# Performance work log

Measured on AMD Instinct MI355X. Metric: run time of the kernel, lower is better.

## Reference

```python
import jax, jax.numpy as jnp
import numpy as np

N_CLASSES = 256
GT_CLASSES = 21
DIM = 384
EPS = 1e-12  # matches torch F.normalize default eps


def setup_inputs() -> dict:
    key = jax.random.key(0)
    k1, k2, k3 = jax.random.split(key, 3)
    features = jax.random.normal(k1, (4, 256, 256, DIM), dtype=jnp.float32)
    weight = jax.random.uniform(k2, (4, 256, 256), dtype=jnp.float32)
    cluster_centers = jax.random.normal(k3, (N_CLASSES, DIM), dtype=jnp.float32)
    pseudo_assignment = (jnp.arange(N_CLASSES) % GT_CLASSES).astype(jnp.int32)
    return {
        "features": features,
        "weight": weight,
        "cluster_centers": cluster_centers,
        "pseudo_assignment": pseudo_assignment,
    }


def _l2norm(x, axis):
    # torch F.normalize: x / max(||x||, eps)
    n = jnp.sqrt(jnp.sum(x * x, axis=axis, keepdims=True))
    return x / jnp.maximum(n, EPS)


def reference(features, weight, cluster_centers, pseudo_assignment):
    lead_shape = features.shape[:-1]
    feats = features.reshape(-1, features.shape[-1])        # [N, D]
    w = weight.reshape(-1)                                   # [N]

    normed_clusters = _l2norm(cluster_centers, axis=1)       # [K, D]
    normed_features = _l2norm(feats, axis=1)                 # [N, D]

    inner_products = normed_features @ normed_clusters.T     # [N, K]
    class_labels = jnp.argmax(inner_products, axis=1)        # [N]

    # -(one_hot(labels) * inner_products).sum(1) == -inner_products[n, labels[n]]
    cluster_loss = -jnp.take_along_axis(
        inner_products, class_labels[:, None], axis=1
    )[:, 0]                                                  # [N]

    loss = jnp.mean(cluster_loss * w)

    pseudo_segs_pred = class_labels.reshape(lead_shape)
    segs_pred = pseudo_assignment[pseudo_segs_pred].astype(jnp.int64)
    return pseudo_segs_pred, segs_pred, loss
```

## Files before the change

kernel.cpp:

```cpp
#include <hip/hip_runtime.h>
#include <hip/hip_bf16.h>

#define NTOT (4*256*256)
#define DIM 384
#define KCL 256
#define BM 64
#define TBS 256
#define GRID_MAIN (NTOT/BM)
#define NT 12
#define EPS 1e-12f

#define AHI    0
#define ALO    4096
#define BH_OFF 8192
#define BL_OFF 24576
#define SMEM_BYTES 40960

typedef __attribute__((ext_vector_type(8))) _Float16 f16x8;
typedef __attribute__((ext_vector_type(4))) float f32x4;

__device__ __forceinline__ void async_copy16(const void* gptr, void* lptr) {
    __builtin_amdgcn_global_load_lds(
        (const __attribute__((address_space(1))) unsigned int*)gptr,
        (__attribute__((address_space(3))) unsigned int*)lptr, 16, 0, 0);
}

__global__ void prep_clusters(const float* __restrict__ cc,
                              _Float16* __restrict__ bh,
                              _Float16* __restrict__ bl) {
    int j = blockIdx.x, l = threadIdx.x;
    float v[6]; float ssq = 0.f;
#pragma unroll
    for (int i = 0; i < 6; ++i) { v[i] = cc[j*DIM + l + 64*i]; ssq = fmaf(v[i], v[i], ssq); }
#pragma unroll
    for (int off = 32; off >= 1; off >>= 1) ssq += __shfl_xor(ssq, off);
    float inv = 1.f / fmaxf(sqrtf(ssq), EPS);
    const int w = j >> 6, n = (j >> 4) & 3, nl = j & 15;
#pragma unroll
    for (int i = 0; i < 6; ++i) {
        int d = l + 64 * i;
        float x = v[i] * inv;
        _Float16 h  = (_Float16)x;
        _Float16 lo = (_Float16)(x - (float)h);
        size_t idx = (size_t)((((((d >> 5)*4 + w)*4 + n)*4 + ((d >> 3) & 3))*16 + nl)*8
                              + (d & 7));
        bh[idx] = h;
        bl[idx] = lo;
    }
}

__global__ __launch_bounds__(TBS, 3)
void kmeans_main(const float* __restrict__ A,
                 const float* __restrict__ W,
                 const _Float16* __restrict__ Bh,
                 const _Float16* __restrict__ Bl,
                 const int*   __restrict__ PA,
                 float* __restrict__ out,
                 float* __restrict__ partial)
{
    __shared__ unsigned char smem[SMEM_BYTES];

    const int tid  = threadIdx.x;
    const int wv   = tid >> 6;
    const int lane = tid & 63;
    const int g    = lane >> 4;
    const int l15  = lane & 15;
    const int sw   = (l15 >> 1) & 3;
    const int row0 = blockIdx.x * BM;
    const int arow = tid >> 2, achk = tid & 3;
    const int awb  = (((arow << 2) + (achk ^ ((arow >> 1) & 3))) << 4);
    const int fa   = l15 * 64 + ((g ^ sw) << 4);
    const int fb   = wv * 4096 + lane * 16;

    const float* ap = A + (size_t)(row0 + arow) * DIM + achk * 8;
    const unsigned char* bsh = (const unsigned char*)Bh + (size_t)(wv * 4) * 1024 + lane * 16;
    const unsigned char* bsl = (const unsigned char*)Bl + (size_t)(wv * 4) * 1024 + lane * 16;

    f32x4 acc[4][4];
#pragma unroll
    for (int m = 0; m < 4; ++m)
#pragma unroll
        for (int n = 0; n < 4; ++n) acc[m][n] = (f32x4){0.f, 0.f, 0.f, 0.f};
    float ssq = 0.f;

    auto stageB = [&](int t) {
#pragma unroll
        for (int n = 0; n < 4; ++n) {
            async_copy16(bsh + (size_t)(t * 16 + n) * 1024, smem + BH_OFF + fb + n * 1024);
            async_copy16(bsl + (size_t)(t * 16 + n) * 1024, smem + BL_OFF + fb + n * 1024);
        }
    };
    auto writeA = [&](const float4& x0, const float4& x1) {
        float av[8] = {x0.x, x0.y, x0.z, x0.w, x1.x, x1.y, x1.z, x1.w};
        f16x8 h8, l8;
#pragma unroll
        for (int e = 0; e < 8; ++e) {
            _Float16 hh = (_Float16)av[e];
            h8[e] = hh;
            l8[e] = (_Float16)(av[e] - (float)hh);
            ssq = fmaf(av[e], av[e], ssq);
        }
        *(f16x8*)(smem + AHI + awb) = h8;
        *(f16x8*)(smem + ALO + awb) = l8;
    };

    float4 rA0x, rA0y, rA1x, rA1y;

    rA0x = *(const float4*)(ap);
    rA0y = *(const float4*)(ap + 4);
    stageB(0);
    writeA(rA0x, rA0y);
    rA1x = *(const float4*)(ap + 32);
    rA1y = *(const float4*)(ap + 32 + 4);
    asm volatile("s_waitcnt lgkmcnt(0)" ::: "memory");
    __builtin_amdgcn_s_barrier();

#pragma unroll
    for (int t = 0; t < NT; ++t) {
        if (t < NT - 1) asm volatile("s_waitcnt vmcnt(2)" ::: "memory");
        else            asm volatile("s_waitcnt vmcnt(0)" ::: "memory");

        f16x8 ahf[4], alf[4], bfh[4], bfl[4];
#pragma unroll
        for (int m = 0; m < 4; ++m) {
            ahf[m] = *(const f16x8*)(smem + AHI + fa + m * 1024);
            alf[m] = *(const f16x8*)(smem + ALO + fa + m * 1024);
        }
#pragma unroll
        for (int n = 0; n < 4; ++n) {
            bfh[n] = *(const f16x8*)(smem + BH_OFF + fb + n * 1024);
            bfl[n] = *(const f16x8*)(smem + BL_OFF + fb + n * 1024);
        }
        asm volatile("s_waitcnt lgkmcnt(0)" ::: "memory");
        __builtin_amdgcn_s_barrier();

        if (t < NT - 1) {
            if (((t + 1) & 1) == 0) writeA(rA0x, rA0y); else writeA(rA1x, rA1y);
            stageB(t + 1);
            if (t + 2 < NT) {
                if (((t + 2) & 1) == 0) {
                    rA0x = *(const float4*)(ap + (t + 2) * 32);
                    rA0y = *(const float4*)(ap + (t + 2) * 32 + 4);
                } else {
                    rA1x = *(const float4*)(ap + (t + 2) * 32);
                    rA1y = *(const float4*)(ap + (t + 2) * 32 + 4);
                }
            }
        }

        __builtin_amdgcn_s_setprio(1);
#pragma unroll
        for (int m = 0; m < 4; ++m)
#pragma unroll
            for (int n = 0; n < 4; ++n)
                acc[m][n] = __builtin_amdgcn_mfma_f32_16x16x32_f16(ahf[m], bfh[n], acc[m][n], 0, 0, 0);
#pragma unroll
        for (int m = 0; m < 4; ++m)
#pragma unroll
            for (int n = 0; n < 4; ++n)
                acc[m][n] = __builtin_amdgcn_mfma_f32_16x16x32_f16(ahf[m], bfl[n], acc[m][n], 0, 0, 0);
#pragma unroll
        for (int m = 0; m < 4; ++m)
#pragma unroll
            for (int n = 0; n < 4; ++n)
                acc[m][n] = __builtin_amdgcn_mfma_f32_16x16x32_f16(alf[m], bfh[n], acc[m][n], 0, 0, 0);
        __builtin_amdgcn_s_setprio(0);

        if (t < NT - 1) {
            asm volatile("s_waitcnt lgkmcnt(0)" ::: "memory");
            __builtin_amdgcn_s_barrier();
        }
    }
    __syncthreads();

    float* rowssq = (float*)smem;
    float* wvalp  = (float*)(smem + 256);
    int*   wcolp  = (int*)(smem + 1280);

    ssq += __shfl_xor(ssq, 1);
    ssq += __shfl_xor(ssq, 2);
    if (achk == 0) rowssq[arow] = ssq;

#pragma unroll
    for (int m = 0; m < 4; ++m) {
#pragma unroll
        for (int j = 0; j < 4; ++j) {
            float best = acc[m][0][j];
            int   bc   = 64*wv + l15;
#pragma unroll
            for (int n = 1; n < 4; ++n) {
                float v = acc[m][n][j];
                int   c = 64*wv + 16*n + l15;
                if (v > best) { best = v; bc = c; }
            }
#pragma unroll
            for (int off = 1; off < 16; off <<= 1) {
                float ov = __shfl_xor(best, off);
                int   oc = __shfl_xor(bc, off);
                if (ov > best || (ov == best && oc < bc)) { best = ov; bc = oc; }
            }
            if (l15 == 0) {
                wvalp[wv * BM + 16*m + 4*g + j] = best;
                wcolp[wv * BM + 16*m + 4*g + j] = bc;
            }
        }
    }
    __syncthreads();

    if (tid < BM) {
        int r = tid;
        float best = wvalp[r]; int bc = wcolp[r];
#pragma unroll
        for (int w = 1; w < 4; ++w) {
            float ov = wvalp[w * BM + r]; int oc = wcolp[w * BM + r];
            if (ov > best || (ov == best && oc < bc)) { best = ov; bc = oc; }
        }
        float inv = 1.f / fmaxf(sqrtf(rowssq[r]), EPS);
        int gr = row0 + r;
        out[gr]        = (float)bc;
        out[NTOT + gr] = (float)PA[bc];
        float lsum = -(best * inv) * W[gr];
#pragma unroll
        for (int off = 32; off >= 1; off >>= 1) lsum += __shfl_xor(lsum, off);
        if (tid == 0) partial[blockIdx.x] = lsum;
    }
}

__global__ void loss_reduce(const float* __restrict__ partial, float* __restrict__ out_loss) {
    __shared__ float s[256];
    float v = 0.f;
    for (int i = threadIdx.x; i < GRID_MAIN; i += 256) v += partial[i];
    s[threadIdx.x] = v;
    __syncthreads();
    for (int off = 128; off >= 1; off >>= 1) {
        if ((int)threadIdx.x < off) s[threadIdx.x] += s[threadIdx.x + off];
        __syncthreads();
    }
    if (threadIdx.x == 0) out_loss[0] = s[0] * (1.0f / (float)NTOT);
}

extern "C" void kernel_launch(void* const* d_in, const int* in_sizes, int n_in,
                              void* d_out, int out_size, void* d_ws, size_t ws_size,
                              hipStream_t stream) {
    const float* features = (const float*)d_in[0];
    const float* weight   = (const float*)d_in[1];
    const float* cc       = (const float*)d_in[2];
    const int*   pa       = (const int*)d_in[3];
    float* out = (float*)d_out;

    _Float16* bh   = (_Float16*)d_ws;
    _Float16* bl   = bh + KCL * DIM;
    float* partial = (float*)(bl + KCL * DIM);

    hipLaunchKernelGGL(prep_clusters, dim3(KCL), dim3(64), 0, stream, cc, bh, bl);
    hipLaunchKernelGGL(kmeans_main, dim3(GRID_MAIN), dim3(TBS), 0, stream,
                       features, weight, bh, bl, pa, out, partial);
    hipLaunchKernelGGL(loss_reduce, dim3(1), dim3(256), 0, stream, partial, out + 2 * NTOT);
}
```

Measured before the change: 202.3 us.

## Load cluster fragments directly to registers and double-buffer A tile in LDS

The B operand (cluster hi/lo fp16 fragments) is no longer staged through LDS via async global-to-LDS copies; each wave loads its fragments straight into registers and prefetches the next tile's B halves between MFMA groups. A is double-buffered in LDS, which removes one barrier per iteration and cuts LDS from 40KB to 16KB. Launch bounds drop from 3 to 2 waves-per-EU minimum to allow the extra registers, which may reduce occupancy, and the direct global loads of B could add latency exposure.

```diff
diff --git a/kernel.cpp b/kernel.cpp
--- a/kernel.cpp
+++ b/kernel.cpp
@@ -10,20 +10,11 @@
 #define NT 12
 #define EPS 1e-12f
 
-#define AHI    0
-#define ALO    4096
-#define BH_OFF 8192
-#define BL_OFF 24576
-#define SMEM_BYTES 40960
+#define AB(p) ((p) * 8192)
+#define SMEM_BYTES 16384
 
 typedef __attribute__((ext_vector_type(8))) _Float16 f16x8;
 typedef __attribute__((ext_vector_type(4))) float f32x4;
-
-__device__ __forceinline__ void async_copy16(const void* gptr, void* lptr) {
-    __builtin_amdgcn_global_load_lds(
-        (const __attribute__((address_space(1))) unsigned int*)gptr,
-        (__attribute__((address_space(3))) unsigned int*)lptr, 16, 0, 0);
-}
 
 __global__ void prep_clusters(const float* __restrict__ cc,
                               _Float16* __restrict__ bh,
@@ -49,7 +40,7 @@
     }
 }
 
-__global__ __launch_bounds__(TBS, 3)
+__global__ __launch_bounds__(TBS, 2)
 void kmeans_main(const float* __restrict__ A,
                  const float* __restrict__ W,
                  const _Float16* __restrict__ Bh,
@@ -70,7 +61,6 @@
     const int arow = tid >> 2, achk = tid & 3;
     const int awb  = (((arow << 2) + (achk ^ ((arow >> 1) & 3))) << 4);
     const int fa   = l15 * 64 + ((g ^ sw) << 4);
-    const int fb   = wv * 4096 + lane * 16;
 
     const float* ap = A + (size_t)(row0 + arow) * DIM + achk * 8;
     const unsigned char* bsh = (const unsigned char*)Bh + (size_t)(wv * 4) * 1024 + lane * 16;
@@ -83,15 +73,26 @@
         for (int n = 0; n < 4; ++n) acc[m][n] = (f32x4){0.f, 0.f, 0.f, 0.f};
     float ssq = 0.f;
 
-    auto stageB = [&](int t) {
-#pragma unroll
-        for (int n = 0; n < 4; ++n) {
-            async_copy16(bsh + (size_t)(t * 16 + n) * 1024, smem + BH_OFF + fb + n * 1024);
-            async_copy16(bsl + (size_t)(t * 16 + n) * 1024, smem + BL_OFF + fb + n * 1024);
-        }
-    };
-    auto writeA = [&](const float4& x0, const float4& x1) {
-        float av[8] = {x0.x, x0.y, x0.z, x0.w, x1.x, x1.y, x1.z, x1.w};
+    f16x8  bfh[4], bfl[4];
+    float4 sA[2][2];
+
+    auto LDA = [&](int s, int tt) {
+        sA[s][0] = *(const float4*)(ap + tt * 32);
+        sA[s][1] = *(const float4*)(ap + tt * 32 + 4);
+    };
+    auto LDBH = [&](int tt) {
+#pragma unroll
+        for (int n = 0; n < 4; ++n)
+            bfh[n] = *(const f16x8*)(bsh + (size_t)(tt * 16 + n) * 1024);
+    };
+    auto LDBL = [&](int tt) {
+#pragma unroll
+        for (int n = 0; n < 4; ++n)
+            bfl[n] = *(const f16x8*)(bsl + (size_t)(tt * 16 + n) * 1024);
+    };
+    auto CVTW = [&](int s, int p) {
+        float av[8] = {sA[s][0].x, sA[s][0].y, sA[s][0].z, sA[s][0].w,
+                       sA[s][1].x, sA[s][1].y, sA[s][1].z, sA[s][1].w};
         f16x8 h8, l8;
 #pragma unroll
         for (int e = 0; e < 8; ++e) {
@@ -100,54 +101,31 @@
             l8[e] = (_Float16)(av[e] - (float)hh);
             ssq = fmaf(av[e], av[e], ssq);
         }
-        *(f16x8*)(smem + AHI + awb) = h8;
-        *(f16x8*)(smem + ALO + awb) = l8;
-    };
-
-    float4 rA0x, rA0y, rA1x, rA1y;
-
-    rA0x = *(const float4*)(ap);
-    rA0y = *(const float4*)(ap + 4);
-    stageB(0);
-    writeA(rA0x, rA0y);
-    rA1x = *(const float4*)(ap + 32);
-    rA1y = *(const float4*)(ap + 32 + 4);
+        *(f16x8*)(smem + AB(p) + awb) = h8;
+        *(f16x8*)(smem + AB(p) + 4096 + awb) = l8;
+    };
+
+    LDA(0, 0);
+    LDBL(0); LDBH(0);
+    LDA(1, 1);
+    CVTW(0, 0);
     asm volatile("s_waitcnt lgkmcnt(0)" ::: "memory");
     __builtin_amdgcn_s_barrier();
 
 #pragma unroll
     for (int t = 0; t < NT; ++t) {
-        if (t < NT - 1) asm volatile("s_waitcnt vmcnt(2)" ::: "memory");
-        else            asm volatile("s_waitcnt vmcnt(0)" ::: "memory");
-
-        f16x8 ahf[4], alf[4], bfh[4], bfl[4];
+        if (t + 2 < NT) LDA((t + 2) & 1, t + 2);
+
+        f16x8 ahf[4], alf[4];
 #pragma unroll
         for (int m = 0; m < 4; ++m) {
-            ahf[m] = *(const f16x8*)(smem + AHI + fa + m * 1024);
-            alf[m] = *(const f16x8*)(smem + ALO + fa + m * 1024);
-        }
-#pragma unroll
-        for (int n = 0; n < 4; ++n) {
-            bfh[n] = *(const f16x8*)(smem + BH_OFF + fb + n * 1024);
-            bfl[n] = *(const f16x8*)(smem + BL_OFF + fb + n * 1024);
-        }
+            ahf[m] = *(const f16x8*)(smem + AB(t & 1) + fa + m * 1024);
+            alf[m] = *(const f16x8*)(smem + AB(t & 1) + 4096 + fa + m * 1024);
+        }
+        if (t + 1 < NT) CVTW((t + 1) & 1, (t + 1) & 1);
         asm volatile("s_waitcnt lgkmcnt(0)" ::: "memory");
         __builtin_amdgcn_s_barrier();
 
-        if (t < NT - 1) {
-            if (((t + 1) & 1) == 0) writeA(rA0x, rA0y); else writeA(rA1x, rA1y);
-            stageB(t + 1);
-            if (t + 2 < NT) {
-                if (((t + 2) & 1) == 0) {
-                    rA0x = *(const float4*)(ap + (t + 2) * 32);
-                    rA0y = *(const float4*)(ap + (t + 2) * 32 + 4);
-                } else {
-                    rA1x = *(const float4*)(ap + (t + 2) * 32);
-                    rA1y = *(const float4*)(ap + (t + 2) * 32 + 4);
-                }
-            }
-        }
-
         __builtin_amdgcn_s_setprio(1);
 #pragma unroll
         for (int m = 0; m < 4; ++m)
@@ -159,17 +137,16 @@
 #pragma unroll
             for (int n = 0; n < 4; ++n)
                 acc[m][n] = __builtin_amdgcn_mfma_f32_16x16x32_f16(ahf[m], bfl[n], acc[m][n], 0, 0, 0);
+        __builtin_amdgcn_s_setprio(0);
+        if (t + 1 < NT) LDBL(t + 1);
+        __builtin_amdgcn_s_setprio(1);
 #pragma unroll
         for (int m = 0; m < 4; ++m)
 #pragma unroll
             for (int n = 0; n < 4; ++n)
                 acc[m][n] = __builtin_amdgcn_mfma_f32_16x16x32_f16(alf[m], bfh[n], acc[m][n], 0, 0, 0);
         __builtin_amdgcn_s_setprio(0);
-
-        if (t < NT - 1) {
-            asm volatile("s_waitcnt lgkmcnt(0)" ::: "memory");
-            __builtin_amdgcn_s_barrier();
-        }
+        if (t + 1 < NT) LDBH(t + 1);
     }
     __syncthreads();
 
```

Result: faster. 182.4 us (-9.8%).
